# Kernel tuning notes

Hardware: AMD Instinct MI355X
Metric: run time of the kernel (lower is better)

## Reference

```python
import jax, jax.numpy as jnp
import numpy as np

N_NODES = 10000
NUM_GENE = 2000
N_EDGES = 160000
HEADS = 10
HID = 128          # GAT layer1 out_channels
LATENT = 128
LOWER = 64
CLUSTERS = 15
SIGMA = 0.5
NEG_SLOPE = 0.2


def gat_conv(x, src, dst, W, a_src, a_dst, b, concat):
    """PyG GATConv (eval mode, self-loops already appended to src/dst).
    x: [N, Fin]; W: [Fin, H*D]; a_src/a_dst: [H, D]; b: [H*D] or [D]."""
    N = x.shape[0]
    H, D = a_src.shape
    h = (x @ W).reshape(N, H, D)                       # [N,H,D]
    e_s = jnp.einsum('nhd,hd->nh', h, a_src)           # [N,H]
    e_d = jnp.einsum('nhd,hd->nh', h, a_dst)
    alpha = jax.nn.leaky_relu(e_s[src] + e_d[dst], NEG_SLOPE)   # [E,H]
    m = jax.ops.segment_max(alpha, dst, num_segments=N)          # [N,H]
    p = jnp.exp(alpha - m[dst])
    s = jax.ops.segment_sum(p, dst, num_segments=N)
    w = p / s[dst]                                     # segment softmax [E,H]
    out = jax.ops.segment_sum(h[src] * w[:, :, None], dst, num_segments=N)  # [N,H,D]
    out = out.reshape(N, H * D) if concat else out.mean(axis=1)
    return out + b


def add_self_loops(edge_index, n):
    loop = jnp.arange(n, dtype=edge_index.dtype)
    src = jnp.concatenate([edge_index[0], loop])
    dst = jnp.concatenate([edge_index[1], loop])
    return src, dst


def setup_inputs() -> dict:
    key = jax.random.key(0)
    ks = jax.random.split(key, 20)
    g = lambda k, shape, fan: jax.random.normal(k, shape, jnp.float32) * (1.0 / np.sqrt(fan))
    inp = {
        'x': jax.random.normal(ks[0], (N_NODES, NUM_GENE), jnp.float32),
        'edge_index': jax.random.randint(ks[1], (2, N_EDGES), 0, N_NODES, dtype=jnp.int32),
        'noise': jax.random.normal(ks[2], (N_NODES, NUM_GENE), jnp.float32) * SIGMA,
        # GAT layer 1: in=NUM_GENE, out=HID, heads=HEADS, concat
        'W1': g(ks[3], (NUM_GENE, HEADS * HID), NUM_GENE),
        'a1_src': g(ks[4], (HEADS, HID), HID),
        'a1_dst': g(ks[5], (HEADS, HID), HID),
        'b1': jnp.zeros((HEADS * HID,), jnp.float32),
        # GAT layer 2: in=HEADS*HID, out=LATENT, heads=HEADS, mean
        'W2': g(ks[6], (HEADS * HID, HEADS * LATENT), HEADS * HID),
        'a2_src': g(ks[7], (HEADS, LATENT), LATENT),
        'a2_dst': g(ks[8], (HEADS, LATENT), LATENT),
        'b2': jnp.zeros((LATENT,), jnp.float32),
        # MLP
        'Wm1': g(ks[9], (NUM_GENE, LATENT), NUM_GENE),
        'bm1': jnp.zeros((LATENT,), jnp.float32),
        'Wm2': g(ks[10], (LATENT, LATENT), LATENT),
        'bm2': jnp.zeros((LATENT,), jnp.float32),
        # projection heads
        'Wf': g(ks[11], (LATENT, LOWER), LATENT),
        'bf': jnp.zeros((LOWER,), jnp.float32),
        'Wc': g(ks[12], (LATENT, CLUSTERS), LATENT),
        'bc': jnp.zeros((CLUSTERS,), jnp.float32),
    }
    return inp


def reference(x, edge_index, noise, W1, a1_src, a1_dst, b1, W2, a2_src, a2_dst, b2,
              Wm1, bm1, Wm2, bm2, Wf, bf, Wc, bc):
    N = x.shape[0]
    src, dst = add_self_loops(edge_index, N)

    # x_aug = x + F.normalize(noise, dim=1)
    nrm = jnp.sqrt(jnp.sum(noise * noise, axis=1, keepdims=True))
    x_aug = x + noise / jnp.maximum(nrm, 1e-12)

    def gat_enc(inp):
        h1 = jax.nn.relu(gat_conv(inp, src, dst, W1, a1_src, a1_dst, b1, concat=True))
        h2 = jax.nn.relu(gat_conv(h1, src, dst, W2, a2_src, a2_dst, b2, concat=False))
        return h2

    gx = gat_enc(x)          # [N, LATENT]
    gx1 = gat_enc(x_aug)
    gx2 = (jax.nn.relu(x @ Wm1 + bm1)) @ Wm2 + bm2   # MLP

    g0 = gx.mean(axis=0)     # global avg pooling -> [LATENT]
    g1 = gx1.mean(axis=0)
    g2 = gx2.mean(axis=0)

    T = 0.2
    e01 = jnp.exp(jnp.dot(g0, g1) / T)
    e02 = jnp.exp(jnp.dot(g0, g2) / T)
    e12 = jnp.exp(jnp.dot(g1, g2) / T)
    loss_graph = -jnp.log10(e01 / (e01 + e02 + e12))

    gx_node = gx @ Wf + bf
    gx1_node = gx1 @ Wf + bf
    gx2_node = gx2 @ Wf + bf
    gx_c = (gx @ Wc + bc).T      # [CLUSTERS, N]
    gx1_c = (gx1 @ Wc + bc).T
    return (gx_node, gx1_node, gx2_node, loss_graph, gx_c, gx1_c)
```

## Files before the change

### kernel.cpp

```cpp
#include <hip/hip_runtime.h>
#include <hip/hip_bf16.h>

#define N_NODESC 10000
#define M_PAD    10112
#define RT_TILES 79
#define NUM_GENE 2000
#define KPAD_G   2048
#define N_EDGESC 160000
#define E_TOT    170000
#define HEADS    10
#define F1       1280
#define LATENTC  128
#define LOWERC   64
#define CLUST    15

typedef __attribute__((ext_vector_type(8))) short   short8;
typedef __attribute__((ext_vector_type(4))) float   f32x4;
typedef __attribute__((ext_vector_type(4))) unsigned short ushort4_;

__device__ __forceinline__ float bf2f(unsigned short u){
    unsigned int x = ((unsigned int)u) << 16;
    return __builtin_bit_cast(float, x);
}
__device__ __forceinline__ unsigned short f2bf(float f){
    __hip_bfloat16 h = __float2bfloat16(f);
    return __builtin_bit_cast(unsigned short, h);
}
__device__ __forceinline__ void gload16(const void* g, void* l) {
    __builtin_amdgcn_global_load_lds((const __attribute__((address_space(1))) void*)g,
                                     (__attribute__((address_space(3))) void*)l, 16, 0, 0);
}

template<int OMODE, int FOLD>
__global__ __launch_bounds__(512, 2)
void gemm256(const unsigned short* __restrict__ A, int lda,
             const unsigned short* __restrict__ BT, int ldb,
             void* __restrict__ Cp, int ldc,
             int NK, int NT, int M_real,
             const float* __restrict__ mbias, unsigned short* __restrict__ mout)
{
    __shared__ short smem[65536];

    const int nwg = gridDim.x;
    const int q = nwg >> 3, r = nwg & 7;
    const int xcd = blockIdx.x & 7, idx = blockIdx.x >> 3;
    const int wgid = (xcd < r ? xcd * (q + 1) : r * (q + 1) + (xcd - r) * q) + idx;
    const int bm = wgid / NT, bn = wgid - bm * NT;

    const int t = threadIdx.x, w = t >> 6, lane = t & 63;
    const int wr2 = (w >> 2) * 64;
    const int wc2 = (w & 3) * 32;
    const int lrow = lane & 15, lq = lane >> 4;

    int rowc[2], swc[2], loff[2];
    #pragma unroll
    for (int cc = 0; cc < 2; ++cc) {
        int c = cc * 512 + t;
        int row = c >> 3, slot = c & 7;
        rowc[cc] = row;
        swc[cc]  = (slot ^ (row & 7)) << 3;
        loff[cc] = c * 8;
    }
    auto stageA = [&](int buf, int h, int kt) {
        short* dst = smem + buf * 32768 + h * 8192;
        const unsigned short* src = A + (size_t)(bm * 256 + h * 128) * lda + kt * 64;
        #pragma unroll
        for (int cc = 0; cc < 2; ++cc)
            gload16(src + (size_t)rowc[cc] * lda + swc[cc], dst + loff[cc]);
    };
    auto stageB = [&](int buf, int h, int kt) {
        short* dst = smem + buf * 32768 + 16384 + h * 8192;
        const unsigned short* src = BT + (size_t)(bn * 256 + h * 128) * ldb + kt * 64;
        #pragma unroll
        for (int cc = 0; cc < 2; ++cc)
            gload16(src + (size_t)rowc[cc] * ldb + swc[cc], dst + loff[cc]);
    };
    auto rdA = [&](int buf, int h, int mi, int ks) -> short8 {
        int r7 = wr2 + mi * 16 + lrow;
        return *(const short8*)(smem + buf * 32768 + h * 8192 + r7 * 64
                                + (((ks * 4 + lq) ^ (r7 & 7)) << 3));
    };
    auto rdB = [&](int buf, int h, int ni, int ks) -> short8 {
        int r7 = wc2 + ni * 16 + lrow;
        return *(const short8*)(smem + buf * 32768 + 16384 + h * 8192 + r7 * 64
                                + (((ks * 4 + lq) ^ (r7 & 7)) << 3));
    };

    f32x4 acc00[4][2] = {}, acc01[4][2] = {}, acc10[4][2] = {}, acc11[4][2] = {};
    short8 a0[4][2], a1[4][2], b0[2][2], b1[2][2];

    auto domfma = [&](f32x4 (&ac)[4][2], short8 (&aa)[4][2], short8 (&bb)[2][2]) {
        __builtin_amdgcn_s_setprio(1);
        #pragma unroll
        for (int mi = 0; mi < 4; ++mi)
            #pragma unroll
            for (int ni = 0; ni < 2; ++ni)
                #pragma unroll
                for (int ks = 0; ks < 2; ++ks)
                    ac[mi][ni] = __builtin_amdgcn_mfma_f32_16x16x32_bf16(
                        aa[mi][ks], bb[ni][ks], ac[mi][ni], 0, 0, 0);
        __builtin_amdgcn_s_setprio(0);
    };

    stageA(0, 0, 0); stageB(0, 0, 0); stageB(0, 1, 0); stageA(0, 1, 0);

    for (int kt = 0; kt < NK; ++kt) {
        const int buf = kt & 1, nbuf = buf ^ 1;
        const bool pf = (kt + 1 < NK);
        asm volatile("s_waitcnt vmcnt(4)" ::: "memory");
        __builtin_amdgcn_sched_barrier(0);
        __builtin_amdgcn_s_barrier();
        __builtin_amdgcn_sched_barrier(0);
        #pragma unroll
        for (int mi = 0; mi < 4; ++mi) { a0[mi][0] = rdA(buf, 0, mi, 0); a0[mi][1] = rdA(buf, 0, mi, 1); }
        #pragma unroll
        for (int ni = 0; ni < 2; ++ni) { b0[ni][0] = rdB(buf, 0, ni, 0); b0[ni][1] = rdB(buf, 0, ni, 1); }
        if (pf) stageA(nbuf, 0, kt + 1);
        domfma(acc00, a0, b0);
        if (pf) { asm volatile("s_waitcnt vmcnt(2)" ::: "memory"); }
        else    { asm volatile("s_waitcnt vmcnt(0)" ::: "memory"); }
        __builtin_amdgcn_sched_barrier(0);
        __builtin_amdgcn_s_barrier();
        __builtin_amdgcn_sched_barrier(0);
        #pragma unroll
        for (int ni = 0; ni < 2; ++ni) { b1[ni][0] = rdB(buf, 1, ni, 0); b1[ni][1] = rdB(buf, 1, ni, 1); }
        if (pf) stageB(nbuf, 0, kt + 1);
        domfma(acc01, a0, b1);
        #pragma unroll
        for (int mi = 0; mi < 4; ++mi) { a1[mi][0] = rdA(buf, 1, mi, 0); a1[mi][1] = rdA(buf, 1, mi, 1); }
        if (pf) stageB(nbuf, 1, kt + 1);
        domfma(acc10, a1, b0);
        if (pf) stageA(nbuf, 1, kt + 1);
        domfma(acc11, a1, b1);
    }

    const bool mlp_tile = FOLD && (bn == NT - 1);
    #pragma unroll
    for (int qa = 0; qa < 2; ++qa) {
        #pragma unroll
        for (int qb = 0; qb < 2; ++qb) {
            f32x4 (&ac)[4][2] = (qa == 0) ? (qb == 0 ? acc00 : acc01)
                                          : (qb == 0 ? acc10 : acc11);
            if (mlp_tile) {
                if (qb != 0) continue;
                #pragma unroll
                for (int mi = 0; mi < 4; ++mi) {
                    #pragma unroll
                    for (int ni = 0; ni < 2; ++ni) {
                        int col = wc2 + ni * 16 + lrow;
                        #pragma unroll
                        for (int qq = 0; qq < 4; ++qq) {
                            int grow = bm * 256 + qa * 128 + wr2 + mi * 16 + lq * 4 + qq;
                            if (grow < N_NODESC) {
                                float val = fmaxf(ac[mi][ni][qq] + mbias[col], 0.f);
                                mout[(size_t)grow * 128 + col] = f2bf(val);
                            }
                        }
                    }
                }
                continue;
            }
            #pragma unroll
            for (int mi = 0; mi < 4; ++mi) {
                #pragma unroll
                for (int ni = 0; ni < 2; ++ni) {
                    int gcol = bn * 256 + qb * 128 + wc2 + ni * 16 + lrow;
                    #pragma unroll
                    for (int qq = 0; qq < 4; ++qq) {
                        int grow = bm * 256 + qa * 128 + wr2 + mi * 16 + lq * 4 + qq;
                        float val = ac[mi][ni][qq];
                        int rslab = grow >= M_PAD ? grow - M_PAD : grow;
                        if (rslab >= M_real) val = 0.f;
                        if constexpr (OMODE == 0)
                            ((unsigned short*)Cp)[(size_t)grow * ldc + gcol] = f2bf(val);
                        else
                            ((float*)Cp)[(size_t)grow * ldc + gcol] = val;
                    }
                }
            }
        }
    }
}

template<int OMODE, int BIAS, int RELU>
__global__ __launch_bounds__(256)
void gemm2(const unsigned short* __restrict__ A, int lda,
           const unsigned short* __restrict__ BT, int ldb,
           const float* __restrict__ bias,
           void* __restrict__ Cp, int ldc,
           int KT, int NT, int M_real)
{
    __shared__ short smem[16384];

    const int nwg = gridDim.x;
    const int q = nwg >> 3, r = nwg & 7;
    const int xcd = blockIdx.x & 7, idx = blockIdx.x >> 3;
    const int wgid = (xcd < r ? xcd * (q + 1) : r * (q + 1) + (xcd - r) * q) + idx;
    const int bm = wgid / NT, bn = wgid - bm * NT;

    const int t = threadIdx.x, w = t >> 6, lane = t & 63;
    const int wr = (w >> 1) * 64, wc = (w & 1) * 64;
    const int lrow = lane & 15, lq = lane >> 4;

    const unsigned short* Ag[2];
    const unsigned short* Bg[2];
    int lds_off[2];
    #pragma unroll
    for (int cc = 0; cc < 2; ++cc) {
        int c = cc * 256 + t;
        int row = c >> 2, slot = c & 3;
        int gk = (slot ^ ((row >> 1) & 3)) << 3;
        Ag[cc] = A  + (size_t)(bm * 128 + row) * lda + gk;
        Bg[cc] = BT + (size_t)(bn * 128 + row) * ldb + gk;
        lds_off[cc] = cc * 2048 + w * 512 + lane * 8;
    }

    auto stage = [&](int buf, int kt) {
        const int kk = kt * 32;
        #pragma unroll
        for (int cc = 0; cc < 2; ++cc) {
            gload16(Ag[cc] + kk, smem + buf * 8192 + lds_off[cc]);
            gload16(Bg[cc] + kk, smem + buf * 8192 + 4096 + lds_off[cc]);
        }
    };

    f32x4 acc[4][4] = {};
    stage(0, 0);
    __syncthreads();
    int cur = 0;
    for (int kt = 0; kt < KT; ++kt) {
        if (kt + 1 < KT) stage(cur ^ 1, kt + 1);
        const short* As = smem + cur * 8192;
        const short* Bs = As + 4096;
        short8 af[4], bf_[4];
        #pragma unroll
        for (int mi = 0; mi < 4; ++mi) {
            int rr = wr + mi * 16 + lrow;
            af[mi] = *(const short8*)(&As[rr * 32 + ((lq ^ ((rr >> 1) & 3)) << 3)]);
        }
        #pragma unroll
        for (int ni = 0; ni < 4; ++ni) {
            int rr = wc + ni * 16 + lrow;
            bf_[ni] = *(const short8*)(&Bs[rr * 32 + ((lq ^ ((rr >> 1) & 3)) << 3)]);
        }
        #pragma unroll
        for (int mi = 0; mi < 4; ++mi)
            #pragma unroll
            for (int ni = 0; ni < 4; ++ni)
                acc[mi][ni] = __builtin_amdgcn_mfma_f32_16x16x32_bf16(af[mi], bf_[ni], acc[mi][ni], 0, 0, 0);
        __syncthreads();
        cur ^= 1;
    }

    #pragma unroll
    for (int mi = 0; mi < 4; ++mi) {
        #pragma unroll
        for (int ni = 0; ni < 4; ++ni) {
            int gcol = bn * 128 + wc + ni * 16 + lrow;
            #pragma unroll
            for (int qq = 0; qq < 4; ++qq) {
                int grow = bm * 128 + wr + mi * 16 + lq * 4 + qq;
                float val = acc[mi][ni][qq];
                if constexpr (BIAS) val += bias[gcol];
                if constexpr (RELU) val = fmaxf(val, 0.f);
                if (grow >= M_real) val = 0.f;
                ((float*)Cp)[(size_t)grow * ldc + gcol] = val;
            }
        }
    }
}

__global__ void convert_both_k(const float* __restrict__ x, const float* __restrict__ noise,
                               unsigned short* __restrict__ out)
{
    __shared__ float sred[4];
    __shared__ float srn;
    int row = blockIdx.x, t = threadIdx.x;
    int kc = t * 8;
    f32x4 n0 = {}, n1 = {};
    float ss = 0.f;
    if (t < 250) {
        n0 = *(const f32x4*)(noise + (size_t)row * NUM_GENE + kc);
        n1 = *(const f32x4*)(noise + (size_t)row * NUM_GENE + kc + 4);
        ss = n0.x*n0.x + n0.y*n0.y + n0.z*n0.z + n0.w*n0.w
           + n1.x*n1.x + n1.y*n1.y + n1.z*n1.z + n1.w*n1.w;
    }
    for (int off = 32; off; off >>= 1) ss += __shfl_down(ss, off);
    if ((t & 63) == 0) sred[t >> 6] = ss;
    __syncthreads();
    if (t == 0) srn = 1.f / fmaxf(sqrtf(sred[0] + sred[1] + sred[2] + sred[3]), 1e-12f);
    __syncthreads();
    if (t >= 250) return;
    float rn = srn;
    f32x4 a0 = *(const f32x4*)(x + (size_t)row * NUM_GENE + kc);
    f32x4 a1 = *(const f32x4*)(x + (size_t)row * NUM_GENE + kc + 4);
    short8 v0, v1;
    #pragma unroll
    for (int i = 0; i < 4; ++i) {
        v0[i]     = (short)f2bf(a0[i]);
        v0[4 + i] = (short)f2bf(a1[i]);
        v1[i]     = (short)f2bf(a0[i] + n0[i] * rn);
        v1[4 + i] = (short)f2bf(a1[i] + n1[i] * rn);
    }
    *(short8*)(out + (size_t)row * KPAD_G + kc) = v0;
    *(short8*)(out + (size_t)(M_PAD + row) * KPAD_G + kc) = v1;
}

__global__ void transpose_bf_k(const float* __restrict__ in, unsigned short* __restrict__ out,
                               int R, int C, int Kpad)
{
    __shared__ float tile[32][33];
    int tx = threadIdx.x & 31, ty = threadIdx.x >> 5;
    int c0 = blockIdx.x * 32, r0 = blockIdx.y * 32;
    #pragma unroll
    for (int i = 0; i < 4; ++i) {
        int r = r0 + ty + i * 8, c = c0 + tx;
        tile[ty + i * 8][tx] = (r < R && c < C) ? in[(size_t)r * C + c] : 0.f;
    }
    __syncthreads();
    #pragma unroll
    for (int i = 0; i < 4; ++i) {
        int c = c0 + ty + i * 8;
        int r = r0 + tx;
        if (c < C && r < Kpad) out[(size_t)c * Kpad + r] = f2bf(tile[tx][ty + i * 8]);
    }
}

__global__ void hist_k(const int* __restrict__ ei, int* __restrict__ cnt)
{
    int e = blockIdx.x * 256 + threadIdx.x;
    if (e >= E_TOT) return;
    int d = (e < N_EDGESC) ? ei[N_EDGESC + e] : (e - N_EDGESC);
    atomicAdd(&cnt[d], 1);
}

__global__ void scan_k(const int* __restrict__ cnt, int* __restrict__ rowp, int* __restrict__ cursor)
{
    __shared__ int buf[1024];
    int t = threadIdx.x;
    int loc[10];
    int s = 0, base = t * 10;
    #pragma unroll
    for (int i = 0; i < 10; ++i) {
        int idx = base + i;
        int v = (idx < N_NODESC) ? cnt[idx] : 0;
        loc[i] = v; s += v;
    }
    buf[t] = s; __syncthreads();
    for (int off = 1; off < 1024; off <<= 1) {
        int tmp = (t >= off) ? buf[t - off] : 0;
        __syncthreads();
        buf[t] += tmp;
        __syncthreads();
    }
    int run = buf[t] - s;
    #pragma unroll
    for (int i = 0; i < 10; ++i) {
        int idx = base + i;
        if (idx < N_NODESC) { rowp[idx] = run; cursor[idx] = run; run += loc[i]; }
    }
    if (t == 1023) rowp[N_NODESC] = buf[1023];
}

__global__ void scatter_k(const int* __restrict__ ei, int* __restrict__ cursor,
                          int* __restrict__ col_src, int* __restrict__ dst_of)
{
    int e = blockIdx.x * 256 + threadIdx.x;
    if (e >= E_TOT) return;
    int s, d;
    if (e < N_EDGESC) { s = ei[e]; d = ei[N_EDGESC + e]; } else { s = d = e - N_EDGESC; }
    int pos = atomicAdd(&cursor[d], 1);
    col_src[pos] = s;
    dst_of[pos] = d;
}

__global__ void escores2_k(const unsigned short* __restrict__ h,
                           const float* __restrict__ a_src, const float* __restrict__ a_dst,
                           float* __restrict__ e_s, float* __restrict__ e_d)
{
    int t = threadIdx.x;
    int half = (t >= 160);
    int tl = t - half * 160;
    int node2 = blockIdx.x * 2 + half;
    int p = node2 >= N_NODESC;
    int n = node2 - p * N_NODESC;
    int hh = tl >> 4, c = tl & 15;
    int off = hh * 128 + c * 8;
    short8 v = *(const short8*)(h + (size_t)(p * M_PAD + n) * F1 + off);
    float ps = 0.f, pd = 0.f;
    #pragma unroll
    for (int j = 0; j < 8; ++j) {
        float f = bf2f((unsigned short)v[j]);
        ps += f * a_src[off + j];
        pd += f * a_dst[off + j];
    }
    #pragma unroll
    for (int m = 1; m < 16; m <<= 1) {
        ps += __shfl_xor(ps, m, 16);
        pd += __shfl_xor(pd, m, 16);
    }
    if (c == 0) { e_s[node2 * HEADS + hh] = ps; e_d[node2 * HEADS + hh] = pd; }
}

__global__ void alpha_k(const int* __restrict__ colsrc, const int* __restrict__ dstof,
                        const float* __restrict__ e_s, const float* __restrict__ e_d,
                        float* __restrict__ alpha)
{
    int gid = blockIdx.x * 256 + threadIdx.x;
    if (gid >= 2 * E_TOT) return;
    int p = gid >= E_TOT;
    int e = gid - p * E_TOT;
    int s = colsrc[e], d = dstof[e];
    const float* er = e_s + (size_t)(p * N_NODESC + s) * HEADS;
    const float* dr = e_d + (size_t)(p * N_NODESC + d) * HEADS;
    #pragma unroll
    for (int h = 0; h < HEADS; ++h) {
        float a = er[h] + dr[h];
        a = a >= 0.f ? a : 0.2f * a;
        alpha[((size_t)p * HEADS + h) * E_TOT + e] = a;
    }
}

__global__ void nodems_k(const int* __restrict__ rowp, const float* __restrict__ alpha,
                         float2* __restrict__ minv)
{
    int gid = blockIdx.x * 256 + threadIdx.x;
    if (gid >= 2 * N_NODESC * HEADS) return;
    int p = gid >= N_NODESC * HEADS;
    int rr = gid - p * N_NODESC * HEADS;
    int n = rr / HEADS, hh = rr - n * HEADS;
    int beg = rowp[n], end = rowp[n + 1];
    const float* ap = alpha + ((size_t)p * HEADS + hh) * E_TOT;
    float m = -1e30f, ssum = 0.f;
    for (int e = beg; e < end; ++e) {
        float a = ap[e];
        if (a > m) { ssum = ssum * __expf(m - a) + 1.f; m = a; }
        else ssum += __expf(a - m);
    }
    float2 qo; qo.x = m; qo.y = 1.f / ssum;
    minv[gid] = qo;
}

__global__ void wexp_k(const int* __restrict__ dstof, const float2* __restrict__ minv,
                       float* __restrict__ alpha)
{
    int gid = blockIdx.x * 256 + threadIdx.x;
    if (gid >= 2 * E_TOT) return;
    int p = gid >= E_TOT;
    int e = gid - p * E_TOT;
    int d = dstof[e];
    const float2* mv = minv + (size_t)(p * N_NODESC + d) * HEADS;
    #pragma unroll
    for (int h = 0; h < HEADS; ++h) {
        float2 qv = mv[h];
        size_t o = ((size_t)p * HEADS + h) * E_TOT + e;
        alpha[o] = __expf(alpha[o] - qv.x) * qv.y;
    }
}

template<int L1MODE>
__global__ void agg_slice_k(const int* __restrict__ rowp, const int* __restrict__ colsrc,
                            const float* __restrict__ alpha,
                            const unsigned short* __restrict__ h,
                            const float* __restrict__ bias,
                            unsigned short* __restrict__ out)
{
    const int nwg = gridDim.x;
    const int q = nwg >> 3, r = nwg & 7;
    const int xcd = blockIdx.x & 7, idx = blockIdx.x >> 3;
    const int wgid = (xcd < r ? xcd * (q + 1) : r * (q + 1) + (xcd - r) * q) + idx;
    int ps = wgid / 625, nb = wgid - ps * 625;
    int p = ps / HEADS, s = ps - p * HEADS;
    int t = threadIdx.x;
    int nl = t >> 4, l16 = t & 15;
    int n = nb * 16 + nl;
    int beg = rowp[n], end = rowp[n + 1];
    const unsigned short* hb = h + (size_t)p * M_PAD * F1 + s * 128 + l16 * 8;
    const float* wb = alpha + ((size_t)p * HEADS + s) * E_TOT;
    float acc[8] = {};
    for (int e = beg; e < end; ++e) {
        int src = colsrc[e];
        float wv = wb[e];
        short8 rv = *(const short8*)(hb + (size_t)src * F1);
        #pragma unroll
        for (int j = 0; j < 8; ++j) acc[j] += wv * bf2f((unsigned short)rv[j]);
    }
    short8 o;
    if constexpr (L1MODE) {
        #pragma unroll
        for (int j = 0; j < 8; ++j)
            o[j] = (short)f2bf(fmaxf(acc[j] + bias[s * 128 + l16 * 8 + j], 0.f));
    } else {
        #pragma unroll
        for (int j = 0; j < 8; ++j) o[j] = (short)f2bf(acc[j]);
    }
    *(short8*)(out + (size_t)(p * M_PAD + n) * F1 + s * 128 + l16 * 8) = o;
}

__global__ void headmean_k(const unsigned short* __restrict__ tmp, const float* __restrict__ b2,
                           float* __restrict__ out)
{
    int gid = blockIdx.x * 256 + threadIdx.x;
    int pn = gid >> 4, d8 = (gid & 15) * 8;
    int p = pn >= N_NODESC;
    int n = pn - p * N_NODESC;
    const unsigned short* tp = tmp + (size_t)(p * M_PAD + n) * F1 + d8;
    float acc[8] = {};
    #pragma unroll
    for (int hh = 0; hh < HEADS; ++hh) {
        short8 v = *(const short8*)(tp + hh * 128);
        #pragma unroll
        for (int j = 0; j < 8; ++j) acc[j] += bf2f((unsigned short)v[j]);
    }
    float* op = out + (size_t)(p * M_PAD + n) * LATENTC + d8;
    #pragma unroll
    for (int j = 0; j < 8; ++j) op[j] = fmaxf(acc[j] * 0.1f + b2[d8 + j], 0.f);
}

__global__ void colsum_k(const float* __restrict__ g01, const float* __restrict__ g2,
                         float* __restrict__ gsum)
{
    int v = blockIdx.x / 40, b = blockIdx.x % 40;
    const float* src = (v == 0) ? g01 : (v == 1) ? g01 + (size_t)M_PAD * 128 : g2;
    int t = threadIdx.x, col = t & 127, ro = t >> 7;
    int rend = min((b + 1) * 250, N_NODESC);
    float acc = 0.f;
    for (int r = b * 250 + ro; r < rend; r += 2) acc += src[(size_t)r * 128 + col];
    __shared__ float part[256];
    part[t] = acc; __syncthreads();
    if (t < 128) atomicAdd(&gsum[v * 128 + col], part[t] + part[t + 128]);
}

__global__ void loss_k(const float* __restrict__ gsum, float* __restrict__ out)
{
    int t = threadIdx.x;
    float g0 = gsum[t] * 1e-4f, g1 = gsum[128 + t] * 1e-4f, g2 = gsum[256 + t] * 1e-4f;
    float d01 = g0 * g1, d02 = g0 * g2, d12 = g1 * g2;
    for (int off = 32; off; off >>= 1) {
        d01 += __shfl_down(d01, off); d02 += __shfl_down(d02, off); d12 += __shfl_down(d12, off);
    }
    __shared__ float s[3][2];
    if ((t & 63) == 0) { int w = t >> 6; s[0][w] = d01; s[1][w] = d02; s[2][w] = d12; }
    __syncthreads();
    if (t == 0) {
        float a01 = (s[0][0] + s[0][1]) * 5.f;
        float a02 = (s[1][0] + s[1][1]) * 5.f;
        float a12 = (s[2][0] + s[2][1]) * 5.f;
        float m = fmaxf(a01, fmaxf(a02, a12));
        float se = expf(a01 - m) + expf(a02 - m) + expf(a12 - m);
        *out = -((a01 - m) - logf(se)) / 2.302585092994046f;
    }
}

__global__ void proj_k(const float* __restrict__ g01, const float* __restrict__ g2,
                       const float* __restrict__ Wf, const float* __restrict__ bfv,
                       const float* __restrict__ Wc, const float* __restrict__ bc,
                       float* __restrict__ out)
{
    __shared__ float rowb[4][128];
    int m = blockIdx.y;
    const float* gx = (m == 0) ? g01 : (m == 1) ? g01 + (size_t)M_PAD * 128 : g2;
    float* out_node = out + (size_t)m * 640000;
    float* out_c = (m == 0) ? out + 1920001 : (m == 1) ? out + 2070001 : nullptr;
    int wid = threadIdx.x >> 6, l = threadIdx.x & 63;
    int n = blockIdx.x * 4 + wid;
    if (n >= N_NODESC) return;
    rowb[wid][l]      = gx[(size_t)n * 128 + l];
    rowb[wid][l + 64] = gx[(size_t)n * 128 + 64 + l];
    float acc = bfv[l];
    #pragma unroll 8
    for (int k = 0; k < 128; ++k) acc += rowb[wid][k] * Wf[k * 64 + l];
    out_node[(size_t)n * 64 + l] = acc;
    if (out_c != nullptr && l < CLUST) {
        float a2 = bc[l];
        #pragma unroll 8
        for (int k = 0; k < 128; ++k) a2 += rowb[wid][k] * Wc[k * CLUST + l];
        out_c[(size_t)l * N_NODESC + n] = a2;
    }
}

extern "C" void kernel_launch(void* const* d_in, const int* in_sizes, int n_in,
                              void* d_out, int out_size, void* d_ws, size_t ws_size,
                              hipStream_t stream)
{
    const float* x     = (const float*)d_in[0];
    const int*   ei    = (const int*)  d_in[1];
    const float* noise = (const float*)d_in[2];
    const float* W1    = (const float*)d_in[3];
    const float* a1s   = (const float*)d_in[4];
    const float* a1d   = (const float*)d_in[5];
    const float* b1    = (const float*)d_in[6];
    const float* W2    = (const float*)d_in[7];
    const float* a2s   = (const float*)d_in[8];
    const float* a2d   = (const float*)d_in[9];
    const float* b2    = (const float*)d_in[10];
    const float* Wm1   = (const float*)d_in[11];
    const float* bm1   = (const float*)d_in[12];
    const float* Wm2   = (const float*)d_in[13];
    const float* bm2   = (const float*)d_in[14];
    const float* Wf    = (const float*)d_in[15];
    const float* bfv   = (const float*)d_in[16];
    const float* Wc    = (const float*)d_in[17];
    const float* bc    = (const float*)d_in[18];
    float* out = (float*)d_out;

    size_t off = 0;
    auto alloc = [&](size_t bytes) { size_t o = off; off = (off + bytes + 255) & ~(size_t)255; return o; };
    char* ws = (char*)d_ws;
    unsigned short* xbuf2  = (unsigned short*)(ws + alloc((size_t)2 * M_PAD * KPAD_G * 2));
    unsigned short* hraw2  = (unsigned short*)(ws + alloc((size_t)2 * M_PAD * F1 * 2));
    unsigned short* w1t    = (unsigned short*)(ws + alloc((size_t)1536 * KPAD_G * 2));
    unsigned short* w2t    = (unsigned short*)(ws + alloc((size_t)F1 * F1 * 2));
    unsigned short* wm2t   = (unsigned short*)(ws + alloc((size_t)128 * 128 * 2));
    unsigned short* t_bf   = (unsigned short*)(ws + alloc((size_t)M_PAD * 128 * 2));
    float*  alpha  = (float*) (ws + alloc((size_t)2 * E_TOT * HEADS * 4));
    float2* minv   = (float2*)(ws + alloc((size_t)2 * N_NODESC * HEADS * 8));
    float*  es     = (float*) (ws + alloc((size_t)2 * N_NODESC * HEADS * 4));
    float*  edv    = (float*) (ws + alloc((size_t)2 * N_NODESC * HEADS * 4));
    int*    cnt    = (int*)   (ws + alloc((size_t)N_NODESC * 4));
    int*    rowp   = (int*)   (ws + alloc((size_t)(N_NODESC + 16) * 4));
    int*    cursor = (int*)   (ws + alloc((size_t)N_NODESC * 4));
    int*    colsrc = (int*)   (ws + alloc((size_t)E_TOT * 4));
    int*    dstof  = (int*)   (ws + alloc((size_t)E_TOT * 4));
    float*  gx01   = (float*) (ws + alloc((size_t)2 * M_PAD * 128 * 4));
    float*  gx2    = (float*) (ws + alloc((size_t)M_PAD * 128 * 4));
    float*  gsum   = (float*) (ws + alloc((size_t)384 * 4));
    unsigned short* h1x2 = xbuf2;
    unsigned short* tmp2 = xbuf2;
    (void)ws_size; (void)in_sizes; (void)n_in; (void)out_size;

    hipMemsetAsync(cnt, 0, (size_t)N_NODESC * 4, stream);
    hipMemsetAsync(gsum, 0, 384 * 4, stream);
    hipMemsetAsync(w1t + (size_t)1408 * KPAD_G, 0, (size_t)128 * KPAD_G * 2, stream);

    convert_both_k<<<N_NODESC, 256, 0, stream>>>(x, noise, xbuf2);

    transpose_bf_k<<<dim3(40, 64), 256, 0, stream>>>(W1,  w1t,  NUM_GENE, F1,  KPAD_G);
    transpose_bf_k<<<dim3(4, 64),  256, 0, stream>>>(Wm1, w1t + (size_t)1280 * KPAD_G, NUM_GENE, 128, KPAD_G);
    transpose_bf_k<<<dim3(40, 40), 256, 0, stream>>>(W2,  w2t,  F1,       F1,  F1);
    transpose_bf_k<<<dim3(4, 4),   256, 0, stream>>>(Wm2, wm2t, 128,      128, 128);

    hist_k   <<<(E_TOT + 255) / 256, 256, 0, stream>>>(ei, cnt);
    scan_k   <<<1, 1024, 0, stream>>>(cnt, rowp, cursor);
    scatter_k<<<(E_TOT + 255) / 256, 256, 0, stream>>>(ei, cursor, colsrc, dstof);

    gemm256<0,1><<<RT_TILES * 6, 512, 0, stream>>>(xbuf2, KPAD_G, w1t, KPAD_G,
        hraw2, F1, 32, 6, N_NODESC, bm1, t_bf);
    gemm2<1,1,0><<<RT_TILES, 256, 0, stream>>>(t_bf, 128, wm2t, 128,
        bm2, gx2, 128, 4, 1, N_NODESC);

    escores2_k<<<N_NODESC, 320, 0, stream>>>(hraw2, a1s, a1d, es, edv);
    alpha_k <<<(2 * E_TOT + 255) / 256, 256, 0, stream>>>(colsrc, dstof, es, edv, alpha);
    nodems_k<<<(2 * N_NODESC * HEADS + 255) / 256, 256, 0, stream>>>(rowp, alpha, minv);
    wexp_k  <<<(2 * E_TOT + 255) / 256, 256, 0, stream>>>(dstof, minv, alpha);
    agg_slice_k<1><<<12500, 256, 0, stream>>>(rowp, colsrc, alpha, hraw2, b1, h1x2);

    gemm256<0,0><<<RT_TILES * 5, 512, 0, stream>>>(h1x2, F1, w2t, F1,
        hraw2, F1, 20, 5, N_NODESC, nullptr, nullptr);
    escores2_k<<<N_NODESC, 320, 0, stream>>>(hraw2, a2s, a2d, es, edv);
    alpha_k <<<(2 * E_TOT + 255) / 256, 256, 0, stream>>>(colsrc, dstof, es, edv, alpha);
    nodems_k<<<(2 * N_NODESC * HEADS + 255) / 256, 256, 0, stream>>>(rowp, alpha, minv);
    wexp_k  <<<(2 * E_TOT + 255) / 256, 256, 0, stream>>>(dstof, minv, alpha);
    agg_slice_k<0><<<12500, 256, 0, stream>>>(rowp, colsrc, alpha, hraw2, nullptr, tmp2);
    headmean_k<<<1250, 256, 0, stream>>>(tmp2, b2, gx01);

    colsum_k<<<120, 256, 0, stream>>>(gx01, gx2, gsum);
    loss_k  <<<1, 128, 0, stream>>>(gsum, out + 1920000);

    proj_k<<<dim3(2500, 3), 256, 0, stream>>>(gx01, gx2, Wf, bfv, Wc, bc, out);
}
```

Baseline: 659.4 us.

## Fuse segment softmax normalize into node pass and reorder GEMM prefetch staging

After: 680.2 us. +3.2%, slower.

```diff
diff --git a/kernel.cpp b/kernel.cpp
--- a/kernel.cpp
+++ b/kernel.cpp
@@ -115,22 +115,21 @@
         for (int mi = 0; mi < 4; ++mi) { a0[mi][0] = rdA(buf, 0, mi, 0); a0[mi][1] = rdA(buf, 0, mi, 1); }
         #pragma unroll
         for (int ni = 0; ni < 2; ++ni) { b0[ni][0] = rdB(buf, 0, ni, 0); b0[ni][1] = rdB(buf, 0, ni, 1); }
-        if (pf) stageA(nbuf, 0, kt + 1);
+        if (pf) { stageA(nbuf, 0, kt + 1); stageB(nbuf, 0, kt + 1); }
         domfma(acc00, a0, b0);
-        if (pf) { asm volatile("s_waitcnt vmcnt(2)" ::: "memory"); }
+        if (pf) { asm volatile("s_waitcnt vmcnt(4)" ::: "memory"); }
         else    { asm volatile("s_waitcnt vmcnt(0)" ::: "memory"); }
         __builtin_amdgcn_sched_barrier(0);
         __builtin_amdgcn_s_barrier();
         __builtin_amdgcn_sched_barrier(0);
         #pragma unroll
         for (int ni = 0; ni < 2; ++ni) { b1[ni][0] = rdB(buf, 1, ni, 0); b1[ni][1] = rdB(buf, 1, ni, 1); }
-        if (pf) stageB(nbuf, 0, kt + 1);
+        if (pf) stageB(nbuf, 1, kt + 1);
         domfma(acc01, a0, b1);
         #pragma unroll
         for (int mi = 0; mi < 4; ++mi) { a1[mi][0] = rdA(buf, 1, mi, 0); a1[mi][1] = rdA(buf, 1, mi, 1); }
-        if (pf) stageB(nbuf, 1, kt + 1);
+        if (pf) stageA(nbuf, 1, kt + 1);
         domfma(acc10, a1, b0);
-        if (pf) stageA(nbuf, 1, kt + 1);
         domfma(acc11, a1, b1);
     }
 
@@ -421,41 +420,24 @@
     }
 }
 
-__global__ void nodems_k(const int* __restrict__ rowp, const float* __restrict__ alpha,
-                         float2* __restrict__ minv)
+__global__ void nodesm_k(const int* __restrict__ rowp, float* __restrict__ alpha)
 {
     int gid = blockIdx.x * 256 + threadIdx.x;
     if (gid >= 2 * N_NODESC * HEADS) return;
     int p = gid >= N_NODESC * HEADS;
     int rr = gid - p * N_NODESC * HEADS;
-    int n = rr / HEADS, hh = rr - n * HEADS;
+    int hh = rr / N_NODESC, n = rr - hh * N_NODESC;
     int beg = rowp[n], end = rowp[n + 1];
-    const float* ap = alpha + ((size_t)p * HEADS + hh) * E_TOT;
+    float* ap = alpha + ((size_t)p * HEADS + hh) * E_TOT;
     float m = -1e30f, ssum = 0.f;
     for (int e = beg; e < end; ++e) {
         float a = ap[e];
         if (a > m) { ssum = ssum * __expf(m - a) + 1.f; m = a; }
         else ssum += __expf(a - m);
     }
-    float2 qo; qo.x = m; qo.y = 1.f / ssum;
-    minv[gid] = qo;
-}
-
-__global__ void wexp_k(const int* __restrict__ dstof, const float2* __restrict__ minv,
-                       float* __restrict__ alpha)
-{
-    int gid = blockIdx.x * 256 + threadIdx.x;
-    if (gid >= 2 * E_TOT) return;
-    int p = gid >= E_TOT;
-    int e = gid - p * E_TOT;
-    int d = dstof[e];
-    const float2* mv = minv + (size_t)(p * N_NODESC + d) * HEADS;
-    #pragma unroll
-    for (int h = 0; h < HEADS; ++h) {
-        float2 qv = mv[h];
-        size_t o = ((size_t)p * HEADS + h) * E_TOT + e;
-        alpha[o] = __expf(alpha[o] - qv.x) * qv.y;
-    }
+    float inv = 1.f / ssum;
+    for (int e = beg; e < end; ++e)
+        ap[e] = __expf(ap[e] - m) * inv;
 }
 
 template<int L1MODE>
@@ -614,7 +596,6 @@
     unsigned short* wm2t   = (unsigned short*)(ws + alloc((size_t)128 * 128 * 2));
     unsigned short* t_bf   = (unsigned short*)(ws + alloc((size_t)M_PAD * 128 * 2));
     float*  alpha  = (float*) (ws + alloc((size_t)2 * E_TOT * HEADS * 4));
-    float2* minv   = (float2*)(ws + alloc((size_t)2 * N_NODESC * HEADS * 8));
     float*  es     = (float*) (ws + alloc((size_t)2 * N_NODESC * HEADS * 4));
     float*  edv    = (float*) (ws + alloc((size_t)2 * N_NODESC * HEADS * 4));
     int*    cnt    = (int*)   (ws + alloc((size_t)N_NODESC * 4));
@@ -651,16 +632,14 @@
 
     escores2_k<<<N_NODESC, 320, 0, stream>>>(hraw2, a1s, a1d, es, edv);
     alpha_k <<<(2 * E_TOT + 255) / 256, 256, 0, stream>>>(colsrc, dstof, es, edv, alpha);
-    nodems_k<<<(2 * N_NODESC * HEADS + 255) / 256, 256, 0, stream>>>(rowp, alpha, minv);
-    wexp_k  <<<(2 * E_TOT + 255) / 256, 256, 0, stream>>>(dstof, minv, alpha);
+    nodesm_k<<<(2 * N_NODESC * HEADS + 255) / 256, 256, 0, stream>>>(rowp, alpha);
     agg_slice_k<1><<<12500, 256, 0, stream>>>(rowp, colsrc, alpha, hraw2, b1, h1x2);
 
     gemm256<0,0><<<RT_TILES * 5, 512, 0, stream>>>(h1x2, F1, w2t, F1,
         hraw2, F1, 20, 5, N_NODESC, nullptr, nullptr);
     escores2_k<<<N_NODESC, 320, 0, stream>>>(hraw2, a2s, a2d, es, edv);
     alpha_k <<<(2 * E_TOT + 255) / 256, 256, 0, stream>>>(colsrc, dstof, es, edv, alpha);
-    nodems_k<<<(2 * N_NODESC * HEADS + 255) / 256, 256, 0, stream>>>(rowp, alpha, minv);
-    wexp_k  <<<(2 * E_TOT + 255) / 256, 256, 0, stream>>>(dstof, minv, alpha);
+    nodesm_k<<<(2 * N_NODESC * HEADS + 255) / 256, 256, 0, stream>>>(rowp, alpha);
     agg_slice_k<0><<<12500, 256, 0, stream>>>(rowp, colsrc, alpha, hraw2, nullptr, tmp2);
     headmean_k<<<1250, 256, 0, stream>>>(tmp2, b2, gx01);
 
```
